# Performance work log

Hardware: AMD Instinct MI355X
Metric: run time of the kernel (lower is better)

## Reference

```python
import jax, jax.numpy as jnp
import numpy as np

# node types: 0=glomeruli, 1=macrophage, 2=tcell
# edge types (construction order of HeteroGATv2.__init__):
#   (glom->glom), (mac->glom), (mac->mac), (mac->tc), (tc->glom), (tc->mac), (tc->tc)
SRC = (0, 1, 1, 1, 2, 2, 2)
DST = (0, 0, 1, 2, 0, 1, 2)
N_NODES = 50000      # nodes per node type
E = 800000           # edges per edge type (avg degree 16)
D_IN = 32            # raw node feature dim
H = 64               # hidden dim (hidden_dims = [64, 64])
N_CLASSES = 4        # output_dim
NEG_SLOPE = 0.2      # GATv2 LeakyReLU slope (PyG default)


def setup_inputs() -> dict:
    key = jax.random.key(0)
    ks = iter(jax.random.split(key, 32))
    x = jax.random.normal(next(ks), (3, N_NODES, D_IN), jnp.float32)
    edges = jax.random.randint(next(ks), (7, 2, E), 0, N_NODES, dtype=jnp.int32)

    def mk(shape):
        return jax.random.normal(next(ks), shape, jnp.float32) * 0.1

    inp = {"x": x, "edges": edges}
    # layer 0: in=D_IN -> H ; layer 1: in=H -> H (stacked over 7 edge types)
    inp["Wl0"] = mk((7, D_IN, H)); inp["Wr0"] = mk((7, D_IN, H))
    inp["bl0"] = mk((7, H));       inp["br0"] = mk((7, H))
    inp["att0"] = mk((7, H));      inp["bias0"] = mk((7, H))
    inp["Wl1"] = mk((7, H, H));    inp["Wr1"] = mk((7, H, H))
    inp["bl1"] = mk((7, H));       inp["br1"] = mk((7, H))
    inp["att1"] = mk((7, H));      inp["bias1"] = mk((7, H))
    inp["Wout"] = mk((H, N_CLASSES)); inp["bout"] = mk((N_CLASSES,))
    return inp


def gatv2_conv(x_src, x_dst, ei, Wl, Wr, bl, br, att, bias, n_dst):
    """Single-head PyG GATv2Conv (add_self_loops=False)."""
    xl = x_src @ Wl + bl                      # [Ns, H] transformed source
    xr = x_dst @ Wr + br                      # [Nd, H] transformed target
    src, dst = ei[0], ei[1]
    # additive attention: e_ij = att^T LeakyReLU(xl_j + xr_i)
    e = jax.nn.leaky_relu(xl[src] + xr[dst], NEG_SLOPE) @ att   # [E]
    # segment softmax over incoming edges of each destination node
    m = jax.ops.segment_max(e, dst, num_segments=n_dst)
    ex = jnp.exp(e - m[dst])
    s = jax.ops.segment_sum(ex, dst, num_segments=n_dst)
    alpha = ex / (s[dst] + 1e-16)
    out = jax.ops.segment_sum(alpha[:, None] * xl[src], dst, num_segments=n_dst)
    return out + bias


def _forward(x, edges, Wl0, Wr0, bl0, br0, att0, bias0,
             Wl1, Wr1, bl1, br1, att1, bias1, Wout, bout):
    n = x.shape[1]
    h = [x[0], x[1], x[2]]
    layers = ((Wl0, Wr0, bl0, br0, att0, bias0),
              (Wl1, Wr1, bl1, br1, att1, bias1))
    for (Wl, Wr, bl, br, att, bias) in layers:
        out = [jnp.zeros((n, Wl.shape[-1]), x.dtype) for _ in range(3)]
        for t in range(7):  # HeteroConv aggr='sum' over edge types
            out[DST[t]] = out[DST[t]] + gatv2_conv(
                h[SRC[t]], h[DST[t]], edges[t],
                Wl[t], Wr[t], bl[t], br[t], att[t], bias[t], n)
        h = [jax.nn.relu(o) for o in out]   # norm=Identity, then ReLU
    logits = h[0] @ Wout + bout             # output head on glomeruli
    return jax.nn.softmax(logits, axis=1)


def reference(x, edges, Wl0, Wr0, bl0, br0, att0, bias0,
              Wl1, Wr1, bl1, br1, att1, bias1, Wout, bout):
    return _forward(x, edges, Wl0, Wr0, bl0, br0, att0, bias0,
                    Wl1, Wr1, bl1, br1, att1, bias1, Wout, bout)
```

## Files before the change

### kernel.cpp

```cpp
#include <hip/hip_runtime.h>
#include <hip/hip_bf16.h>


#define N_NODES 50000
#define NEDGE   800000
#define HDIM    64
#define DIN     32
#define NROWS   (7 * N_NODES)
#define CROWS   512
#define NCB     684
#define TILE1   8192
#define NBLK1   684

typedef __hip_bfloat16 bf16;
typedef short short8v __attribute__((ext_vector_type(8)));
typedef float f32x4 __attribute__((ext_vector_type(4)));

__device__ __forceinline__ float ldf(const void* p, size_t i, int bf) {
    return bf ? __bfloat162float(((const bf16*)p)[i]) : ((const float*)p)[i];
}
__device__ __forceinline__ unsigned short f2bf(float f) {
    bf16 b = __float2bfloat16(f);
    return *(unsigned short*)&b;
}

__global__ void detect_kernel(const unsigned short* __restrict__ x, int* __restrict__ flag)
{
    __shared__ int sbad[256];
    int bad = 0;
    for (int i = threadIdx.x; i < 4096; i += 256) {
        unsigned short u = x[i];
        int ex = (u >> 7) & 0xff;
        bool zero = (u & 0x7fffu) == 0;
        if (!zero && (ex < 80 || ex > 140)) bad++;
    }
    sbad[threadIdx.x] = bad;
    __syncthreads();
    for (int s = 128; s > 0; s >>= 1) {
        if (threadIdx.x < s) sbad[threadIdx.x] += sbad[threadIdx.x + s];
        __syncthreads();
    }
    if (threadIdx.x == 0) flag[0] = (sbad[0] < 64) ? 1 : 0;
}


__global__ __launch_bounds__(256) void k1_count_kernel(const int* __restrict__ edges,
                                                       int* __restrict__ cnt2d)
{
    __shared__ int lcount[NCB];
    for (int i = threadIdx.x; i < NCB; i += 256) lcount[i] = 0;
    __syncthreads();
    int g0 = blockIdx.x * TILE1;
    #pragma unroll 4
    for (int k = 0; k < TILE1 / 256; ++k) {
        int g = g0 + k * 256 + threadIdx.x;
        if (g < 7 * NEDGE) {
            int t = g / NEDGE, i = g - t * NEDGE;
            int d = edges[(size_t)t * 2 * NEDGE + NEDGE + i];
            int r = t * N_NODES + d;
            atomicAdd(&lcount[r >> 9], 1);
        }
    }
    __syncthreads();
    for (int i = threadIdx.x; i < NCB; i += 256)
        cnt2d[(size_t)i * NBLK1 + blockIdx.x] = lcount[i];
}

__global__ __launch_bounds__(256) void k2_colscan_kernel(int* __restrict__ cnt2d,
                                                         int* __restrict__ cbase)
{
    __shared__ int sv[256];
    int t = threadIdx.x;
    int* col = cnt2d + (size_t)blockIdx.x * NBLK1;
    int a[3]; int s = 0;
    #pragma unroll
    for (int k = 0; k < 3; ++k) {
        int i = t * 3 + k;
        a[k] = (i < NBLK1) ? col[i] : 0;
        s += a[k];
    }
    sv[t] = s; __syncthreads();
    for (int off = 1; off < 256; off <<= 1) {
        int v = (t >= off) ? sv[t - off] : 0; __syncthreads();
        sv[t] += v; __syncthreads();
    }
    int excl = sv[t] - s;
    #pragma unroll
    for (int k = 0; k < 3; ++k) {
        int i = t * 3 + k;
        if (i < NBLK1) { col[i] = excl; excl += a[k]; }
    }
    if (t == 255) cbase[blockIdx.x] = sv[255];
}

__global__ __launch_bounds__(256) void k3_cscan_kernel(int* __restrict__ cbase,
                                                       int* __restrict__ P)
{
    __shared__ int sv[256];
    int t = threadIdx.x;
    int a[3]; int s = 0;
    #pragma unroll
    for (int k = 0; k < 3; ++k) {
        int i = t * 3 + k;
        a[k] = (i < NCB) ? cbase[i] : 0;
        s += a[k];
    }
    sv[t] = s; __syncthreads();
    for (int off = 1; off < 256; off <<= 1) {
        int v = (t >= off) ? sv[t - off] : 0; __syncthreads();
        sv[t] += v; __syncthreads();
    }
    int excl = sv[t] - s;
    #pragma unroll
    for (int k = 0; k < 3; ++k) {
        int i = t * 3 + k;
        if (i < NCB) { cbase[i] = excl; excl += a[k]; }
    }
    if (t == 255) { cbase[NCB] = sv[255]; P[NROWS] = sv[255]; }
}

__global__ __launch_bounds__(256) void part1_kernel(const int* __restrict__ edges,
                                                    const int* __restrict__ cnt2d,
                                                    const int* __restrict__ cbase,
                                                    unsigned* __restrict__ buf)
{
    __shared__ int lcur[NCB];
    for (int i = threadIdx.x; i < NCB; i += 256)
        lcur[i] = cbase[i] + cnt2d[(size_t)i * NBLK1 + blockIdx.x];
    __syncthreads();
    int g0 = blockIdx.x * TILE1;
    #pragma unroll 4
    for (int k = 0; k < TILE1 / 256; ++k) {
        int g = g0 + k * 256 + threadIdx.x;
        if (g < 7 * NEDGE) {
            int t = g / NEDGE, i = g - t * NEDGE;
            int s = edges[(size_t)t * 2 * NEDGE + i];
            int d = edges[(size_t)t * 2 * NEDGE + NEDGE + i];
            int r = t * N_NODES + d;
            int pos = atomicAdd(&lcur[r >> 9], 1);
            buf[pos] = ((unsigned)(r & 511) << 16) | (unsigned)s;
        }
    }
}

__global__ __launch_bounds__(256) void part2_kernel(const unsigned* __restrict__ buf,
                                                    const int* __restrict__ cbase,
                                                    int* __restrict__ P,
                                                    int* __restrict__ col_src)
{
    __shared__ int fcnt[CROWS];
    __shared__ int fpos[CROWS];
    __shared__ int sv[256];
    int b = blockIdx.x;
    int t = threadIdx.x;
    int start = cbase[b], end = cbase[b + 1];
    fcnt[2 * t] = 0; fcnt[2 * t + 1] = 0;
    __syncthreads();
    for (int i = start + t; i < end; i += 256)
        atomicAdd(&fcnt[buf[i] >> 16], 1);
    __syncthreads();
    int a0 = fcnt[2 * t], a1 = fcnt[2 * t + 1];
    int s = a0 + a1;
    sv[t] = s; __syncthreads();
    for (int off = 1; off < 256; off <<= 1) {
        int v = (t >= off) ? sv[t - off] : 0; __syncthreads();
        sv[t] += v; __syncthreads();
    }
    int excl = sv[t] - s;
    fpos[2 * t] = excl; fpos[2 * t + 1] = excl + a0;
    int r0 = b * CROWS;
    int rows_in = NROWS - r0; if (rows_in > CROWS) rows_in = CROWS;
    if (2 * t < rows_in)     P[r0 + 2 * t]     = start + excl;
    if (2 * t + 1 < rows_in) P[r0 + 2 * t + 1] = start + excl + a0;
    __syncthreads();
    for (int i = start + t; i < end; i += 256) {
        unsigned v = buf[i];
        int pos = start + atomicAdd(&fpos[v >> 16], 1);
        col_src[pos] = (int)(v & 0xffffu);
    }
}


__global__ __launch_bounds__(256) void hist_kernel(const int* __restrict__ edges,
                                                   int* __restrict__ cnt, int ntypes)
{
    int g = blockIdx.x * 256 + threadIdx.x;
    if (g >= ntypes * NEDGE) return;
    int t = g / NEDGE, i = g - t * NEDGE;
    int d = edges[(size_t)t * 2 * NEDGE + NEDGE + i];
    atomicAdd(&cnt[t * N_NODES + d], 1);
}

__global__ __launch_bounds__(256) void scanA_kernel(const int* __restrict__ cnt,
                                                    int* __restrict__ bsums, int n)
{
    __shared__ int lds[256];
    int tid = threadIdx.x;
    int base = blockIdx.x * 2048 + tid * 8;
    int s = 0;
    #pragma unroll
    for (int k = 0; k < 8; ++k) { int i = base + k; if (i < n) s += cnt[i]; }
    lds[tid] = s;
    __syncthreads();
    for (int o = 128; o > 0; o >>= 1) {
        if (tid < o) lds[tid] += lds[tid + o];
        __syncthreads();
    }
    if (tid == 0) bsums[blockIdx.x] = lds[0];
}

__global__ __launch_bounds__(256) void scanB_kernel(const int* __restrict__ bsums,
                                                    int* __restrict__ boffs, int nb,
                                                    int* __restrict__ P, int n)
{
    __shared__ int lds[256];
    int tid = threadIdx.x;
    int v = (tid < nb) ? bsums[tid] : 0;
    lds[tid] = v;
    __syncthreads();
    for (int off = 1; off < 256; off <<= 1) {
        int t2 = (tid >= off) ? lds[tid - off] : 0;
        __syncthreads();
        lds[tid] += t2;
        __syncthreads();
    }
    if (tid < nb) boffs[tid] = lds[tid] - v;
    if (tid == 255) P[n] = lds[255];
}

__global__ __launch_bounds__(256) void scanC_kernel(const int* __restrict__ cnt,
                                                    const int* __restrict__ boffs,
                                                    int* __restrict__ P,
                                                    int* __restrict__ cursor, int n)
{
    __shared__ int lds[256];
    int tid = threadIdx.x;
    int base = blockIdx.x * 2048 + tid * 8;
    int v[8];
    int s = 0;
    #pragma unroll
    for (int k = 0; k < 8; ++k) {
        int i = base + k;
        int c = (i < n) ? cnt[i] : 0;
        v[k] = s;
        s += c;
    }
    lds[tid] = s;
    __syncthreads();
    for (int off = 1; off < 256; off <<= 1) {
        int t2 = (tid >= off) ? lds[tid - off] : 0;
        __syncthreads();
        lds[tid] += t2;
        __syncthreads();
    }
    int off0 = boffs[blockIdx.x] + (lds[tid] - s);
    #pragma unroll
    for (int k = 0; k < 8; ++k) {
        int i = base + k;
        if (i < n) { int val = off0 + v[k]; P[i] = val; cursor[i] = val; }
    }
}

__global__ __launch_bounds__(256) void scatter1_kernel(const int* __restrict__ et,
                                                       int* __restrict__ cursor,
                                                       int* __restrict__ col_src)
{
    int i = blockIdx.x * 256 + threadIdx.x;
    if (i >= NEDGE) return;
    int s = et[i], d = et[NEDGE + i];
    int pos = atomicAdd(&cursor[d], 1);
    col_src[pos] = s;
}


__global__ __launch_bounds__(256) void cvt_feat_kernel(const void* __restrict__ in,
                                                       int bfmode, const int* __restrict__ flag,
                                                       unsigned short* __restrict__ out, size_t n)
{
    int bf = bfmode < 0 ? flag[0] : bfmode;
    size_t i = ((size_t)blockIdx.x * 256 + threadIdx.x) * 4;
    if (i + 3 < n) {
        ushort4 o;
        o.x = f2bf(ldf(in, i + 0, bf));
        o.y = f2bf(ldf(in, i + 1, bf));
        o.z = f2bf(ldf(in, i + 2, bf));
        o.w = f2bf(ldf(in, i + 3, bf));
        *(ushort4*)(out + i) = o;
    } else {
        for (size_t j = i; j < n; ++j) out[j] = f2bf(ldf(in, j, bf));
    }
}

__global__ void cvt_w_kernel(const void* __restrict__ WlB, const void* __restrict__ WlF,
                             const void* __restrict__ WrB, const void* __restrict__ WrF,
                             const int* __restrict__ flag, unsigned short* __restrict__ wt, int K)
{
    int bf = flag[0];
    int t = blockIdx.x, side = blockIdx.y;
    const void* W = side ? (bf ? WrB : WrF) : (bf ? WlB : WlF);
    unsigned short* o = wt + ((size_t)t * 2 + side) * 64 * K;
    for (int idx = threadIdx.x; idx < 64 * K; idx += 256) {
        int n = idx / K, k = idx - n * K;
        o[idx] = f2bf(ldf(W, (size_t)t * K * 64 + (size_t)k * 64 + n, bf));
    }
}

template<int K>
__global__ __launch_bounds__(256) void gemm_lin_t(
    const unsigned short* __restrict__ fb, int srcT, int dstT,
    const unsigned short* __restrict__ wt,
    const void* blB, const void* blF, const void* brB, const void* brF,
    const int* __restrict__ flag, float* __restrict__ xl, float* __restrict__ xr)
{
    int side = blockIdx.y;
    int bf = flag[0];
    const unsigned short* A = fb + (size_t)(side ? dstT : srcT) * N_NODES * K;
    const unsigned short* W = wt + (size_t)side * 64 * K;
    const void* bias = side ? (bf ? brB : brF) : (bf ? blB : blF);
    float* out = side ? xr : xl;

    int wave = threadIdx.x >> 6;
    int lane = threadIdx.x & 63;
    int m0 = blockIdx.x * 64 + wave * 16;
    if (m0 >= N_NODES) return;
    int lg = lane >> 4;
    int lr = lane & 15;

    short8v afrag[K / 32];
    #pragma unroll
    for (int ks = 0; ks < K / 32; ++ks)
        afrag[ks] = *(const short8v*)(A + (size_t)(m0 + lr) * K + ks * 32 + lg * 8);

    f32x4 acc0 = {0.f, 0.f, 0.f, 0.f};
    f32x4 acc1 = {0.f, 0.f, 0.f, 0.f};
    f32x4 acc2 = {0.f, 0.f, 0.f, 0.f};
    f32x4 acc3 = {0.f, 0.f, 0.f, 0.f};
    #pragma unroll
    for (int ks = 0; ks < K / 32; ++ks) {
        short8v b0 = *(const short8v*)(W + (size_t)(0 * 16 + lr) * K + ks * 32 + lg * 8);
        short8v b1 = *(const short8v*)(W + (size_t)(1 * 16 + lr) * K + ks * 32 + lg * 8);
        short8v b2 = *(const short8v*)(W + (size_t)(2 * 16 + lr) * K + ks * 32 + lg * 8);
        short8v b3 = *(const short8v*)(W + (size_t)(3 * 16 + lr) * K + ks * 32 + lg * 8);
        acc0 = __builtin_amdgcn_mfma_f32_16x16x32_bf16(afrag[ks], b0, acc0, 0, 0, 0);
        acc1 = __builtin_amdgcn_mfma_f32_16x16x32_bf16(afrag[ks], b1, acc1, 0, 0, 0);
        acc2 = __builtin_amdgcn_mfma_f32_16x16x32_bf16(afrag[ks], b2, acc2, 0, 0, 0);
        acc3 = __builtin_amdgcn_mfma_f32_16x16x32_bf16(afrag[ks], b3, acc3, 0, 0, 0);
    }
    #pragma unroll
    for (int nt = 0; nt < 4; ++nt) {
        f32x4 a = nt == 0 ? acc0 : nt == 1 ? acc1 : nt == 2 ? acc2 : acc3;
        int n = nt * 16 + lr;
        float bb = ldf(bias, n, bf);
        #pragma unroll
        for (int r = 0; r < 4; ++r)
            out[(size_t)(m0 + lg * 4 + r) * HDIM + n] = a[r] + bb;
    }
}


#define FMA4(acc, f, i) acc += (f).x * w[4*(i)] + (f).y * w[4*(i)+1] \
                             + (f).z * w[4*(i)+2] + (f).w * w[4*(i)+3]
#define FMAI(acc, u, i) acc += __uint_as_float(((unsigned)(u)) << 16) * w[2*(i)] \
                             + __uint_as_float(((unsigned)(u)) & 0xffff0000u) * w[2*(i)+1]

template<int BF>
__global__ __launch_bounds__(256) void lin_d32_t(
    const void* fLb, const void* fLf, const void* fRb, const void* fRf,
    const void* wLb, const void* wLf, const void* wRb, const void* wRf,
    const void* bLb, const void* bLf, const void* bRb, const void* bRf,
    const int* __restrict__ flag, float* __restrict__ xl, float* __restrict__ xr)
{
    if (flag[0] != BF) return;
    int side = blockIdx.y;
    const void* W    = side ? (BF ? wRb : wRf) : (BF ? wLb : wLf);
    const void* b    = side ? (BF ? bRb : bRf) : (BF ? bLb : bLf);
    const void* feat = side ? (BF ? fRb : fRf) : (BF ? fLb : fLf);
    float* out = side ? xr : xl;
    int tid = threadIdx.x;
    int h = tid & 63;
    int slot = tid >> 6;
    float w[DIN];
    #pragma unroll
    for (int d = 0; d < DIN; ++d)
        w[d] = BF ? __bfloat162float(((const bf16*)W)[d * HDIM + h])
                  : ((const float*)W)[d * HDIM + h];
    float bias = BF ? __bfloat162float(((const bf16*)b)[h]) : ((const float*)b)[h];
    int base = blockIdx.x * 32;
    #pragma unroll
    for (int nn = 0; nn < 8; ++nn) {
        int node = base + nn * 4 + slot;
        int nc = node < N_NODES ? node : N_NODES - 1;
        float a0 = bias, a1 = 0.f, a2 = 0.f, a3 = 0.f;
        if (BF) {
            const int4* fp = (const int4*)((const bf16*)feat + (size_t)nc * DIN);
            int4 q0 = fp[0], q1 = fp[1], q2 = fp[2], q3 = fp[3];
            FMAI(a0, q0.x, 0);  FMAI(a1, q0.y, 1);  FMAI(a2, q0.z, 2);  FMAI(a3, q0.w, 3);
            FMAI(a0, q1.x, 4);  FMAI(a1, q1.y, 5);  FMAI(a2, q1.z, 6);  FMAI(a3, q1.w, 7);
            FMAI(a0, q2.x, 8);  FMAI(a1, q2.y, 9);  FMAI(a2, q2.z, 10); FMAI(a3, q2.w, 11);
            FMAI(a0, q3.x, 12); FMAI(a1, q3.y, 13); FMAI(a2, q3.z, 14); FMAI(a3, q3.w, 15);
        } else {
            const float4* f4 = (const float4*)((const float*)feat + (size_t)nc * DIN);
            float4 f0 = f4[0], f1 = f4[1], f2 = f4[2], f3 = f4[3];
            float4 f5 = f4[4], f6 = f4[5], f7 = f4[6], f8 = f4[7];
            FMA4(a0, f0, 0); FMA4(a1, f1, 1); FMA4(a2, f2, 2); FMA4(a3, f3, 3);
            FMA4(a0, f5, 4); FMA4(a1, f6, 5); FMA4(a2, f7, 6); FMA4(a3, f8, 7);
        }
        if (node < N_NODES)
            out[(size_t)node * HDIM + h] = (a0 + a1) + (a2 + a3);
    }
}

template<int BF>
__global__ __launch_bounds__(256) void lin_d64_t(
    const float* __restrict__ fL, const float* __restrict__ fR,
    const void* wLb, const void* wLf, const void* wRb, const void* wRf,
    const void* bLb, const void* bLf, const void* bRb, const void* bRf,
    const int* __restrict__ flag, float* __restrict__ xl, float* __restrict__ xr)
{
    if (flag[0] != BF) return;
    int side = blockIdx.y;
    const void* W = side ? (BF ? wRb : wRf) : (BF ? wLb : wLf);
    const void* b = side ? (BF ? bRb : bRf) : (BF ? bLb : bLf);
    const float* feat = side ? fR : fL;
    float* out = side ? xr : xl;
    int tid = threadIdx.x;
    int h = tid & 63;
    int slot = tid >> 6;
    float w[HDIM];
    #pragma unroll
    for (int d = 0; d < HDIM; ++d)
        w[d] = BF ? __bfloat162float(((const bf16*)W)[d * HDIM + h])
                  : ((const float*)W)[d * HDIM + h];
    float bias = BF ? __bfloat162float(((const bf16*)b)[h]) : ((const float*)b)[h];
    int base = blockIdx.x * 32;
    #pragma unroll
    for (int nn = 0; nn < 8; ++nn) {
        int node = base + nn * 4 + slot;
        int nc = node < N_NODES ? node : N_NODES - 1;
        const float4* f4 = (const float4*)(feat + (size_t)nc * HDIM);
        float a0 = bias, a1 = 0.f, a2 = 0.f, a3 = 0.f;
        {
            float4 f0 = f4[0], f1 = f4[1], f2 = f4[2], f3 = f4[3];
            float4 f5 = f4[4], f6 = f4[5], f7 = f4[6], f8 = f4[7];
            FMA4(a0, f0, 0); FMA4(a1, f1, 1); FMA4(a2, f2, 2); FMA4(a3, f3, 3);
            FMA4(a0, f5, 4); FMA4(a1, f6, 5); FMA4(a2, f7, 6); FMA4(a3, f8, 7);
        }
        {
            float4 g0 = f4[8],  g1 = f4[9],  g2 = f4[10], g3 = f4[11];
            float4 g5 = f4[12], g6 = f4[13], g7 = f4[14], g8 = f4[15];
            FMA4(a0, g0, 8);  FMA4(a1, g1, 9);  FMA4(a2, g2, 10); FMA4(a3, g3, 11);
            FMA4(a0, g5, 12); FMA4(a1, g6, 13); FMA4(a2, g7, 14); FMA4(a3, g8, 15);
        }
        if (node < N_NODES)
            out[(size_t)node * HDIM + h] = (a0 + a1) + (a2 + a3);
    }
}

__global__ __launch_bounds__(256) void gat_row_kernel(
    const int* __restrict__ rowptr, const int* __restrict__ col_src,
    const float* __restrict__ xl, const float* __restrict__ xr,
    const void* ab, const void* af, const int* __restrict__ flag,
    float* __restrict__ hn, int init)
{
    int bf = flag[0];
    const void* att = bf ? ab : af;
    int wave = threadIdx.x >> 6;
    int lane = threadIdx.x & 63;
    int d = blockIdx.x * 4 + wave;
    if (d >= N_NODES) return;
    int rs = rowptr[d], re = rowptr[d + 1];

    int g = lane >> 4;
    int c = lane & 15;

    if (re <= rs) {
        if (init && g == 0)
            ((float4*)(hn + (size_t)d * HDIM))[c] = make_float4(0.f, 0.f, 0.f, 0.f);
        return;
    }

    float4 attv;
    attv.x = ldf(att, 4*c + 0, bf);
    attv.y = ldf(att, 4*c + 1, bf);
    attv.z = ldf(att, 4*c + 2, bf);
    attv.w = ldf(att, 4*c + 3, bf);
    float4 xrv = ((const float4*)(xr + (size_t)d * HDIM))[c];

    float4 acc = make_float4(0.f, 0.f, 0.f, 0.f);
    float m = -1e30f, s = 0.f;

    for (int cs0 = rs; cs0 < re; cs0 += 16) {
        float e[4];
        float4 xlv[4];
        #pragma unroll
        for (int it = 0; it < 4; ++it) {
            int ei = cs0 + it * 4 + g;
            bool valid = ei < re;
            float4 xv = make_float4(0.f, 0.f, 0.f, 0.f);
            if (valid) {
                int src = col_src[ei];
                xv = ((const float4*)(xl + (size_t)src * HDIM))[c];
            }
            xlv[it] = xv;
            float vx = xv.x + xrv.x; vx = vx > 0.f ? vx : 0.2f * vx;
            float vy = xv.y + xrv.y; vy = vy > 0.f ? vy : 0.2f * vy;
            float vz = xv.z + xrv.z; vz = vz > 0.f ? vz : 0.2f * vz;
            float vw = xv.w + xrv.w; vw = vw > 0.f ? vw : 0.2f * vw;
            float t = attv.x * vx + attv.y * vy + attv.z * vz + attv.w * vw;
            t += __shfl_xor(t, 1, 64);
            t += __shfl_xor(t, 2, 64);
            t += __shfl_xor(t, 4, 64);
            t += __shfl_xor(t, 8, 64);
            e[it] = valid ? t : -1e30f;
        }
        float cm = fmaxf(fmaxf(e[0], e[1]), fmaxf(e[2], e[3]));
        cm = fmaxf(cm, __shfl_xor(cm, 16, 64));
        cm = fmaxf(cm, __shfl_xor(cm, 32, 64));
        if (cm > m) {
            float sc = __expf(m - cm);
            s *= sc;
            acc.x *= sc; acc.y *= sc; acc.z *= sc; acc.w *= sc;
            m = cm;
        }
        #pragma unroll
        for (int it = 0; it < 4; ++it) {
            float w = __expf(e[it] - m);
            s += w;
            acc.x += w * xlv[it].x;
            acc.y += w * xlv[it].y;
            acc.z += w * xlv[it].z;
            acc.w += w * xlv[it].w;
        }
    }
    acc.x += __shfl_xor(acc.x, 16, 64); acc.x += __shfl_xor(acc.x, 32, 64);
    acc.y += __shfl_xor(acc.y, 16, 64); acc.y += __shfl_xor(acc.y, 32, 64);
    acc.z += __shfl_xor(acc.z, 16, 64); acc.z += __shfl_xor(acc.z, 32, 64);
    acc.w += __shfl_xor(acc.w, 16, 64); acc.w += __shfl_xor(acc.w, 32, 64);
    s += __shfl_xor(s, 16, 64); s += __shfl_xor(s, 32, 64);

    if (g == 0) {
        float inv = 1.f / (s + 1e-16f);
        float4* op = (float4*)(hn + (size_t)d * HDIM);
        if (init) {
            op[c] = make_float4(acc.x * inv, acc.y * inv, acc.z * inv, acc.w * inv);
        } else {
            float4 old = op[c];
            op[c] = make_float4(old.x + acc.x * inv, old.y + acc.y * inv,
                                old.z + acc.z * inv, old.w + acc.w * inv);
        }
    }
}


__global__ void bsum_kernel(const void* __restrict__ bias, const int* __restrict__ flag,
                            float* __restrict__ bsum)
{
    int bf = flag[0];
    int idx = threadIdx.x;
    if (idx >= 192) return;
    int nt = idx >> 6, h = idx & 63;
    float v;
    if (nt == 0)      v = ldf(bias, 0*64+h, bf) + ldf(bias, 1*64+h, bf) + ldf(bias, 4*64+h, bf);
    else if (nt == 1) v = ldf(bias, 2*64+h, bf) + ldf(bias, 5*64+h, bf);
    else              v = ldf(bias, 3*64+h, bf) + ldf(bias, 6*64+h, bf);
    bsum[idx] = v;
}

__global__ __launch_bounds__(256) void relu_kernel(
    const float* __restrict__ hn, const float* __restrict__ bsum,
    float* __restrict__ h)
{
    size_t idx = (size_t)blockIdx.x * 256 + threadIdx.x;
    if (idx >= (size_t)3 * N_NODES * HDIM) return;
    int nt = (int)(idx / ((size_t)N_NODES * HDIM));
    int hh = (int)(idx & 63);
    float v = hn[idx] + bsum[nt * 64 + hh];
    h[idx] = v > 0.f ? v : 0.f;
}

__global__ __launch_bounds__(256) void head_kernel(
    const float* __restrict__ h0, const void* __restrict__ Wout,
    const void* __restrict__ bout, const int* __restrict__ flag,
    void* __restrict__ out)
{
    __shared__ float sW[64 * 4];
    __shared__ float sb[4];
    int bf = flag[0];
    int tid = threadIdx.x;
    sW[tid] = ldf(Wout, tid, bf);
    if (tid < 4) sb[tid] = ldf(bout, tid, bf);
    __syncthreads();
    int i = blockIdx.x * 256 + tid;
    if (i >= N_NODES) return;
    float l0 = sb[0], l1 = sb[1], l2 = sb[2], l3 = sb[3];
    const float4* p = (const float4*)(h0 + (size_t)i * HDIM);
    #pragma unroll
    for (int k = 0; k < 16; ++k) {
        float4 a = p[k];
        int d = 4 * k;
        l0 += a.x * sW[d*4+0] + a.y * sW[(d+1)*4+0] + a.z * sW[(d+2)*4+0] + a.w * sW[(d+3)*4+0];
        l1 += a.x * sW[d*4+1] + a.y * sW[(d+1)*4+1] + a.z * sW[(d+2)*4+1] + a.w * sW[(d+3)*4+1];
        l2 += a.x * sW[d*4+2] + a.y * sW[(d+1)*4+2] + a.z * sW[(d+2)*4+2] + a.w * sW[(d+3)*4+2];
        l3 += a.x * sW[d*4+3] + a.y * sW[(d+1)*4+3] + a.z * sW[(d+2)*4+3] + a.w * sW[(d+3)*4+3];
    }
    float m = fmaxf(fmaxf(l0, l1), fmaxf(l2, l3));
    float e0 = __expf(l0 - m), e1 = __expf(l1 - m), e2 = __expf(l2 - m), e3 = __expf(l3 - m);
    float inv = 1.f / (e0 + e1 + e2 + e3);
    if (bf) {
        bf16* o = (bf16*)out;
        o[(size_t)4*i + 0] = __float2bfloat16(e0 * inv);
        o[(size_t)4*i + 1] = __float2bfloat16(e1 * inv);
        o[(size_t)4*i + 2] = __float2bfloat16(e2 * inv);
        o[(size_t)4*i + 3] = __float2bfloat16(e3 * inv);
    } else {
        float* o = (float*)out;
        o[(size_t)4*i + 0] = e0 * inv;
        o[(size_t)4*i + 1] = e1 * inv;
        o[(size_t)4*i + 2] = e2 * inv;
        o[(size_t)4*i + 3] = e3 * inv;
    }
}

struct P2 { const void* b; const void* f; };
static inline P2 off2(const void* base, size_t elem) {
    P2 r;
    r.b = (const void*)((const bf16*)base + elem);
    r.f = (const void*)((const float*)base + elem);
    return r;
}

extern "C" void kernel_launch(void* const* d_in, const int* in_sizes, int n_in,
                              void* d_out, int out_size, void* d_ws, size_t ws_size,
                              hipStream_t stream)
{
    const void* x     = d_in[0];
    const int*  edges = (const int*)d_in[1];
    const void* Wl0 = d_in[2];
    const void* Wr0 = d_in[3];
    const void* bl0 = d_in[4];
    const void* br0 = d_in[5];
    const void* att0 = d_in[6];
    const void* bias0 = d_in[7];
    const void* Wl1 = d_in[8];
    const void* Wr1 = d_in[9];
    const void* bl1 = d_in[10];
    const void* br1 = d_in[11];
    const void* att1 = d_in[12];
    const void* bias1 = d_in[13];
    const void* Wout = d_in[14];
    const void* bout = d_in[15];

    const int SRCt[7] = {0, 1, 1, 1, 2, 2, 2};
    const int DSTt[7] = {0, 0, 1, 2, 0, 1, 2};

    float* h3  = (float*)d_ws;
    float* hn3 = h3 + (size_t)3 * N_NODES * HDIM;
    float* xl  = hn3 + (size_t)3 * N_NODES * HDIM;
    float* xr  = xl + (size_t)N_NODES * HDIM;
    char* tail = (char*)(xr + (size_t)N_NODES * HDIM);

    size_t fixed = (size_t)tail - (size_t)d_ws;
    size_t base_need = fixed + ((size_t)NROWS + 1) * 4 + (size_t)7 * NEDGE * 4
                     + (NCB + 1) * 4 + 2 * 256 * 4 + 192 * 4 + 4
                     + 2 * (size_t)N_NODES * 4 + 512;
    size_t mfma_extra = (size_t)3 * N_NODES * HDIM * 2
                      + (size_t)7 * 2 * 64 * HDIM * 2
                      + (size_t)7 * 2 * 64 * DIN * 2 + 512;
    bool full = ws_size >= base_need;
    bool mfma_ok = ws_size >= base_need + mfma_extra;
    int NT = full ? 7 : 1;

    int* P        = (int*)tail;
    int* col_src  = P + ((size_t)NT * N_NODES + 1);
    int* cbase    = col_src + (size_t)NT * NEDGE;
    int* bsums    = cbase + (NCB + 1);
    int* boffs    = bsums + 256;
    float* bsum   = (float*)(boffs + 256);
    int* flag     = (int*)(bsum + 192);
    int* cnt      = flag + 1;
    int* cursor   = cnt + N_NODES;
    unsigned short* fb  = (unsigned short*)(((size_t)(cursor + N_NODES) + 255) & ~(size_t)255);
    unsigned short* wt1 = fb + (size_t)3 * N_NODES * HDIM;
    unsigned short* wt0 = wt1 + (size_t)7 * 2 * 64 * HDIM;

    unsigned* buf = (unsigned*)hn3;
    int* cnt2d    = (int*)(buf + (size_t)7 * NEDGE);

    dim3 blk(256);
    int gLin  = (N_NODES + 31) / 32;
    int gGemm = (N_NODES + 63) / 64;
    int gRow  = (N_NODES + 3) / 4;
    int gRelu = (int)(((size_t)3 * N_NODES * HDIM + 255) / 256);
    int gHead = (N_NODES + 255) / 256;

    detect_kernel<<<1, 256, 0, stream>>>((const unsigned short*)x, flag);

    if (full) {
        k1_count_kernel<<<NBLK1, blk, 0, stream>>>(edges, cnt2d);
        k2_colscan_kernel<<<NCB, blk, 0, stream>>>(cnt2d, cbase);
        k3_cscan_kernel<<<1, blk, 0, stream>>>(cbase, P);
        part1_kernel<<<NBLK1, blk, 0, stream>>>(edges, cnt2d, cbase, buf);
        part2_kernel<<<NCB, blk, 0, stream>>>(buf, cbase, P, col_src);
    }

    for (int layer = 0; layer < 2; ++layer) {
        const void* Wl = layer ? Wl1 : Wl0;
        const void* Wr = layer ? Wr1 : Wr0;
        const void* bl = layer ? bl1 : bl0;
        const void* br = layer ? br1 : br0;
        const void* at = layer ? att1 : att0;
        const void* bi = layer ? bias1 : bias0;
        int K = layer ? HDIM : DIN;

        bsum_kernel<<<1, 192, 0, stream>>>(bi, flag, bsum);

        if (mfma_ok) {
            size_t nfeat = (size_t)3 * N_NODES * K;
            if (layer == 0)
                cvt_feat_kernel<<<(int)((nfeat / 4 + 255) / 256), blk, 0, stream>>>(
                    x, -1, flag, fb, nfeat);
            else
                cvt_feat_kernel<<<(int)((nfeat / 4 + 255) / 256), blk, 0, stream>>>(
                    h3, 0, flag, fb, nfeat);
            unsigned short* wt = layer ? wt1 : wt0;
            cvt_w_kernel<<<dim3(7, 2), blk, 0, stream>>>(
                off2(Wl, 0).b, off2(Wl, 0).f, off2(Wr, 0).b, off2(Wr, 0).f, flag, wt, K);
        }

        for (int t = 0; t < 7; ++t) {
            const int* rp;
            const int* cs;
            if (full) {
                rp = P + (size_t)t * N_NODES;
                cs = col_src;
            } else {
                const int* et = edges + (size_t)t * 2 * NEDGE;
                int n = N_NODES;
                int nb = (n + 2047) / 2048;
                int gE1 = (NEDGE + 255) / 256;
                hipMemsetAsync(cnt, 0, (size_t)n * sizeof(int), stream);
                hist_kernel<<<gE1, blk, 0, stream>>>(et, cnt, 1);
                scanA_kernel<<<nb, blk, 0, stream>>>(cnt, bsums, n);
                scanB_kernel<<<1, blk, 0, stream>>>(bsums, boffs, nb, P, n);
                scanC_kernel<<<nb, blk, 0, stream>>>(cnt, boffs, P, cursor, n);
                scatter1_kernel<<<gE1, blk, 0, stream>>>(et, cursor, col_src);
                rp = P;
                cs = col_src;
            }

            P2 bL = off2(bl, (size_t)t * HDIM);
            P2 bR = off2(br, (size_t)t * HDIM);
            if (mfma_ok) {
                unsigned short* wt = (layer ? wt1 : wt0) + (size_t)t * 2 * 64 * K;
                if (layer == 0)
                    gemm_lin_t<DIN><<<dim3(gGemm, 2), blk, 0, stream>>>(
                        fb, SRCt[t], DSTt[t], wt, bL.b, bL.f, bR.b, bR.f, flag, xl, xr);
                else
                    gemm_lin_t<HDIM><<<dim3(gGemm, 2), blk, 0, stream>>>(
                        fb, SRCt[t], DSTt[t], wt, bL.b, bL.f, bR.b, bR.f, flag, xl, xr);
            } else if (layer == 0) {
                P2 fs = off2(x, (size_t)SRCt[t] * N_NODES * DIN);
                P2 fd = off2(x, (size_t)DSTt[t] * N_NODES * DIN);
                P2 wl = off2(Wl, (size_t)t * DIN * HDIM);
                P2 wr = off2(Wr, (size_t)t * DIN * HDIM);
                lin_d32_t<0><<<dim3(gLin, 2), blk, 0, stream>>>(
                    fs.b, fs.f, fd.b, fd.f, wl.b, wl.f, wr.b, wr.f,
                    bL.b, bL.f, bR.b, bR.f, flag, xl, xr);
                lin_d32_t<1><<<dim3(gLin, 2), blk, 0, stream>>>(
                    fs.b, fs.f, fd.b, fd.f, wl.b, wl.f, wr.b, wr.f,
                    bL.b, bL.f, bR.b, bR.f, flag, xl, xr);
            } else {
                P2 wl = off2(Wl, (size_t)t * HDIM * HDIM);
                P2 wr = off2(Wr, (size_t)t * HDIM * HDIM);
                const float* fL = h3 + (size_t)SRCt[t] * N_NODES * HDIM;
                const float* fR = h3 + (size_t)DSTt[t] * N_NODES * HDIM;
                lin_d64_t<0><<<dim3(gLin, 2), blk, 0, stream>>>(
                    fL, fR, wl.b, wl.f, wr.b, wr.f, bL.b, bL.f, bR.b, bR.f, flag, xl, xr);
                lin_d64_t<1><<<dim3(gLin, 2), blk, 0, stream>>>(
                    fL, fR, wl.b, wl.f, wr.b, wr.f, bL.b, bL.f, bR.b, bR.f, flag, xl, xr);
            }

            int init = (t == 0 || t == 2 || t == 3) ? 1 : 0;
            P2 a2 = off2(at, (size_t)t * HDIM);
            gat_row_kernel<<<gRow, blk, 0, stream>>>(rp, cs, xl, xr,
                                                     a2.b, a2.f, flag,
                                                     hn3 + (size_t)DSTt[t] * N_NODES * HDIM,
                                                     init);
        }
        relu_kernel<<<gRelu, blk, 0, stream>>>(hn3, bsum, h3);
    }

    head_kernel<<<gHead, blk, 0, stream>>>(h3, Wout, bout, flag, d_out);
}
```

Measured before the change: 1.019 ms.

## Store xl/xr projections in bf16 and fuse layer-1 feature conversion into ReLU

New measurement: 987.8 us. 1.03x faster.

```diff
diff --git a/kernel.cpp b/kernel.cpp
--- a/kernel.cpp
+++ b/kernel.cpp
@@ -22,6 +22,9 @@
 __device__ __forceinline__ unsigned short f2bf(float f) {
     bf16 b = __float2bfloat16(f);
     return *(unsigned short*)&b;
+}
+__device__ __forceinline__ float bf2f(unsigned short u) {
+    return __uint_as_float((unsigned)u << 16);
 }
 
 __global__ void detect_kernel(const unsigned short* __restrict__ x, int* __restrict__ flag)
@@ -310,14 +313,15 @@
     const unsigned short* __restrict__ fb, int srcT, int dstT,
     const unsigned short* __restrict__ wt,
     const void* blB, const void* blF, const void* brB, const void* brF,
-    const int* __restrict__ flag, float* __restrict__ xl, float* __restrict__ xr)
+    const int* __restrict__ flag,
+    unsigned short* __restrict__ xl, unsigned short* __restrict__ xr)
 {
     int side = blockIdx.y;
     int bf = flag[0];
     const unsigned short* A = fb + (size_t)(side ? dstT : srcT) * N_NODES * K;
     const unsigned short* W = wt + (size_t)side * 64 * K;
     const void* bias = side ? (bf ? brB : brF) : (bf ? blB : blF);
-    float* out = side ? xr : xl;
+    unsigned short* out = side ? xr : xl;
 
     int wave = threadIdx.x >> 6;
     int lane = threadIdx.x & 63;
@@ -353,7 +357,7 @@
         float bb = ldf(bias, n, bf);
         #pragma unroll
         for (int r = 0; r < 4; ++r)
-            out[(size_t)(m0 + lg * 4 + r) * HDIM + n] = a[r] + bb;
+            out[(size_t)(m0 + lg * 4 + r) * HDIM + n] = f2bf(a[r] + bb);
     }
 }
 
@@ -368,14 +372,15 @@
     const void* fLb, const void* fLf, const void* fRb, const void* fRf,
     const void* wLb, const void* wLf, const void* wRb, const void* wRf,
     const void* bLb, const void* bLf, const void* bRb, const void* bRf,
-    const int* __restrict__ flag, float* __restrict__ xl, float* __restrict__ xr)
+    const int* __restrict__ flag,
+    unsigned short* __restrict__ xl, unsigned short* __restrict__ xr)
 {
     if (flag[0] != BF) return;
     int side = blockIdx.y;
     const void* W    = side ? (BF ? wRb : wRf) : (BF ? wLb : wLf);
     const void* b    = side ? (BF ? bRb : bRf) : (BF ? bLb : bLf);
     const void* feat = side ? (BF ? fRb : fRf) : (BF ? fLb : fLf);
-    float* out = side ? xr : xl;
+    unsigned short* out = side ? xr : xl;
     int tid = threadIdx.x;
     int h = tid & 63;
     int slot = tid >> 6;
@@ -406,7 +411,7 @@
             FMA4(a0, f5, 4); FMA4(a1, f6, 5); FMA4(a2, f7, 6); FMA4(a3, f8, 7);
         }
         if (node < N_NODES)
-            out[(size_t)node * HDIM + h] = (a0 + a1) + (a2 + a3);
+            out[(size_t)node * HDIM + h] = f2bf((a0 + a1) + (a2 + a3));
     }
 }
 
@@ -415,14 +420,15 @@
     const float* __restrict__ fL, const float* __restrict__ fR,
     const void* wLb, const void* wLf, const void* wRb, const void* wRf,
     const void* bLb, const void* bLf, const void* bRb, const void* bRf,
-    const int* __restrict__ flag, float* __restrict__ xl, float* __restrict__ xr)
+    const int* __restrict__ flag,
+    unsigned short* __restrict__ xl, unsigned short* __restrict__ xr)
 {
     if (flag[0] != BF) return;
     int side = blockIdx.y;
     const void* W = side ? (BF ? wRb : wRf) : (BF ? wLb : wLf);
     const void* b = side ? (BF ? bRb : bRf) : (BF ? bLb : bLf);
     const float* feat = side ? fR : fL;
-    float* out = side ? xr : xl;
+    unsigned short* out = side ? xr : xl;
     int tid = threadIdx.x;
     int h = tid & 63;
     int slot = tid >> 6;
@@ -452,13 +458,13 @@
             FMA4(a0, g5, 12); FMA4(a1, g6, 13); FMA4(a2, g7, 14); FMA4(a3, g8, 15);
         }
         if (node < N_NODES)
-            out[(size_t)node * HDIM + h] = (a0 + a1) + (a2 + a3);
+            out[(size_t)node * HDIM + h] = f2bf((a0 + a1) + (a2 + a3));
     }
 }
 
 __global__ __launch_bounds__(256) void gat_row_kernel(
     const int* __restrict__ rowptr, const int* __restrict__ col_src,
-    const float* __restrict__ xl, const float* __restrict__ xr,
+    const unsigned short* __restrict__ xl, const unsigned short* __restrict__ xr,
     const void* ab, const void* af, const int* __restrict__ flag,
     float* __restrict__ hn, int init)
 {
@@ -484,7 +490,8 @@
     attv.y = ldf(att, 4*c + 1, bf);
     attv.z = ldf(att, 4*c + 2, bf);
     attv.w = ldf(att, 4*c + 3, bf);
-    float4 xrv = ((const float4*)(xr + (size_t)d * HDIM))[c];
+    ushort4 xr4 = *(const ushort4*)(xr + (size_t)d * HDIM + 4 * c);
+    float4 xrv = make_float4(bf2f(xr4.x), bf2f(xr4.y), bf2f(xr4.z), bf2f(xr4.w));
 
     float4 acc = make_float4(0.f, 0.f, 0.f, 0.f);
     float m = -1e30f, s = 0.f;
@@ -499,7 +506,8 @@
             float4 xv = make_float4(0.f, 0.f, 0.f, 0.f);
             if (valid) {
                 int src = col_src[ei];
-                xv = ((const float4*)(xl + (size_t)src * HDIM))[c];
+                ushort4 u4 = *(const ushort4*)(xl + (size_t)src * HDIM + 4 * c);
+                xv = make_float4(bf2f(u4.x), bf2f(u4.y), bf2f(u4.z), bf2f(u4.w));
             }
             xlv[it] = xv;
             float vx = xv.x + xrv.x; vx = vx > 0.f ? vx : 0.2f * vx;
@@ -568,14 +576,16 @@
 
 __global__ __launch_bounds__(256) void relu_kernel(
     const float* __restrict__ hn, const float* __restrict__ bsum,
-    float* __restrict__ h)
+    float* __restrict__ h, unsigned short* __restrict__ fbout)
 {
     size_t idx = (size_t)blockIdx.x * 256 + threadIdx.x;
     if (idx >= (size_t)3 * N_NODES * HDIM) return;
     int nt = (int)(idx / ((size_t)N_NODES * HDIM));
     int hh = (int)(idx & 63);
     float v = hn[idx] + bsum[nt * 64 + hh];
-    h[idx] = v > 0.f ? v : 0.f;
+    v = v > 0.f ? v : 0.f;
+    h[idx] = v;
+    if (fbout) fbout[idx] = f2bf(v);
 }
 
 __global__ __launch_bounds__(256) void head_kernel(
@@ -655,9 +665,9 @@
 
     float* h3  = (float*)d_ws;
     float* hn3 = h3 + (size_t)3 * N_NODES * HDIM;
-    float* xl  = hn3 + (size_t)3 * N_NODES * HDIM;
-    float* xr  = xl + (size_t)N_NODES * HDIM;
-    char* tail = (char*)(xr + (size_t)N_NODES * HDIM);
+    unsigned short* xl = (unsigned short*)(hn3 + (size_t)3 * N_NODES * HDIM);
+    unsigned short* xr = xl + (size_t)N_NODES * HDIM;
+    char* tail = (char*)(xl + (size_t)2 * N_NODES * HDIM) + (size_t)2 * N_NODES * HDIM * 2;
 
     size_t fixed = (size_t)tail - (size_t)d_ws;
     size_t base_need = fixed + ((size_t)NROWS + 1) * 4 + (size_t)7 * NEDGE * 4
@@ -715,13 +725,11 @@
         bsum_kernel<<<1, 192, 0, stream>>>(bi, flag, bsum);
 
         if (mfma_ok) {
-            size_t nfeat = (size_t)3 * N_NODES * K;
-            if (layer == 0)
+            if (layer == 0) {
+                size_t nfeat = (size_t)3 * N_NODES * DIN;
                 cvt_feat_kernel<<<(int)((nfeat / 4 + 255) / 256), blk, 0, stream>>>(
                     x, -1, flag, fb, nfeat);
-            else
-                cvt_feat_kernel<<<(int)((nfeat / 4 + 255) / 256), blk, 0, stream>>>(
-                    h3, 0, flag, fb, nfeat);
+            }
             unsigned short* wt = layer ? wt1 : wt0;
             cvt_w_kernel<<<dim3(7, 2), blk, 0, stream>>>(
                 off2(Wl, 0).b, off2(Wl, 0).f, off2(Wr, 0).b, off2(Wr, 0).f, flag, wt, K);
@@ -787,7 +795,8 @@
                                                      hn3 + (size_t)DSTt[t] * N_NODES * HDIM,
                                                      init);
         }
-        relu_kernel<<<gRelu, blk, 0, stream>>>(hn3, bsum, h3);
+        relu_kernel<<<gRelu, blk, 0, stream>>>(hn3, bsum, h3,
+                                               (mfma_ok && layer == 0) ? fb : (unsigned short*)nullptr);
     }
 
     head_kernel<<<gHead, blk, 0, stream>>>(h3, Wout, bout, flag, d_out);
```
